# Kernel tuning notes

Measured on AMD Instinct MI355X. Metric: run time of the kernel, lower is better.

## Reference

```python
import jax, jax.numpy as jnp
import numpy as np

# --- fan-beam (flat detector) FBP geometry constants, matching init geo dict ---
V, U = 720, 736            # sino_views, nDetecU
NX = NY = 512              # nVoxelX, nVoxelY
SVOX = 400.0               # sVoxelX = sVoxelY (mm)
DU = 1.2858                # dDetecU (mm)
DSO, DOD = 595.0, 490.6    # source-origin, origin-detector distances
DSD = DSO + DOD
DBETA = 2.0 * np.pi / V    # angular step (full 2*pi scan, endpoint=False)


def _ramp_filter_fft():
    """Ram-Lak ramp filter (Kak & Slaney discrete spatial kernel), FFT'd for fast conv."""
    n = np.arange(-(U - 1), U)
    h = np.zeros(2 * U - 1, np.float64)
    h[U - 1] = 1.0 / (4.0 * DU * DU)
    odd = (np.abs(n) % 2 == 1)
    h[odd] = -1.0 / (np.pi * n[odd] * DU) ** 2
    L = int(2 ** np.ceil(np.log2(2 * (2 * U - 1))))  # zero-pad length (linear conv)
    return jnp.asarray(np.fft.fft(h, L).astype(np.complex64)), L

_HF, _L = _ramp_filter_fft()


def setup_inputs() -> dict:
    key = jax.random.key(0)
    sinogram = jax.random.uniform(key, (1, 1, V, U), dtype=jnp.float32)
    return {"sinogram": sinogram}


def reference(sinogram):
    # --- 1) cosine weighting of each detector sample ---
    sino = sinogram.reshape(V, U)
    us = (jnp.arange(U, dtype=jnp.float32) - (U - 1) / 2.0) * DU  # detector coords
    sino_w = sino * (DSD / jnp.sqrt(DSD * DSD + us * us))

    # --- 2) Ram-Lak ramp filtering per view (FFT linear convolution) ---
    Qf = jnp.fft.ifft(jnp.fft.fft(sino_w, n=_L, axis=1) * _HF[None, :], axis=1)
    Q = (jnp.real(Qf)[:, U - 1:2 * U - 1] * DU).astype(jnp.float32)  # [V, U]

    # --- 3) weighted fan-beam backprojection (scan over angles, O(Nx*Ny) carry) ---
    dx = SVOX / NX
    xs = (jnp.arange(NX, dtype=jnp.float32) - (NX - 1) / 2.0) * dx
    X, Y = jnp.meshgrid(xs, xs, indexing='ij')  # [NX, NY]
    betas = jnp.linspace(0.0, 2.0 * np.pi, V, endpoint=False).astype(jnp.float32)

    def body(img, ang_q):
        beta, q = ang_q                       # q: filtered projection [U]
        cb, sb = jnp.cos(beta), jnp.sin(beta)
        t = X * cb + Y * sb                   # coord along detector direction
        s = -X * sb + Y * cb                  # coord toward source
        D = DSO - s                           # source-to-pixel axial distance
        u = DSD * t / D                       # flat-detector intersection (mm)
        idx = u / DU + (U - 1) / 2.0          # fractional detector index
        i0 = jnp.clip(jnp.floor(idx), 0, U - 2).astype(jnp.int32)
        f = idx - i0
        val = q[i0] * (1.0 - f) + q[i0 + 1] * f
        val = jnp.where((idx >= 0.0) & (idx <= U - 1.0), val, 0.0)
        return img + (DSO / D) ** 2 * val, None

    img0 = jnp.zeros((NX, NY), jnp.float32)
    img, _ = jax.lax.scan(body, img0, (betas, Q))
    # 0.5 factor: full 2*pi fan scan covers each ray twice
    return (img * (0.5 * DBETA)).reshape(1, 1, NX, NY)
```

## Files before the change

kernel.cpp:

```cpp
#include <hip/hip_runtime.h>
#include <math.h>

#define NV 720
#define NU 736
#define NUP 768
#define NXY 512

__global__ __launch_bounds__(512) void filter_kernel(const float* __restrict__ sino,
                                                     float* __restrict__ Qi,
                                                     float4* __restrict__ trig,
                                                     float* __restrict__ out_zero) {
    __shared__ float s4[2][368][4];
    __shared__ float wco[736];
    __shared__ float part[3][128][8];
    const int bx = blockIdx.x;
    const int q = bx & 3;
    const int vb = bx >> 2;
    const int v0 = vb * 4;
    const int tid = threadIdx.x;
    const int tz = tid >> 7;
    const int J0 = tid & 127;

    for (int i = bx * 512 + tid; i < NXY * NXY; i += 720 * 512)
        out_zero[i] = 0.0f;

    if (q == 0 && tid < 4) {
        int v = v0 + tid;
        float beta = (float)((double)v * (2.0 * M_PI / 720.0));
        float cb = cosf(beta), sb = sinf(beta);
        const float K = (float)(1085.6 / 1.2858);
        trig[v] = make_float4(cb * K, sb * K, cb, sb);
    }
    const float DSD2 = (float)(1085.6 * 1085.6);
    for (int i = tid; i < 4 * NU; i += 512) {
        const int vv = i / NU, u = i - vv * NU;
        float us = ((float)u - 367.5f) * 1.2858f;
        float cw = 1085.6f / sqrtf(DSD2 + us * us);
        s4[u & 1][u >> 1][vv] = sino[(v0 + vv) * NU + u] * cw;
    }
    for (int i = tid; i < 736; i += 512) {
        double n = (double)(2 * i - 735);
        double a = M_PI * n * 1.2858;
        wco[i] = (float)(-1.0 / (a * a));
    }
    __syncthreads();

    const int m0 = 92 * tz;
    float a00 = 0.f, a01 = 0.f, a02 = 0.f, a03 = 0.f;
    float a10 = 0.f, a11 = 0.f, a12 = 0.f, a13 = 0.f;
    const int J0c = min(J0, 91);
    const int y0 = J0c + 367 + 92 * q;
    const float* wp = &wco[y0 - m0];

    #pragma unroll 4
    for (int mm = 0; mm < 92; ++mm) {
        const int m = m0 + mm;
        const float w0 = wp[-mm];
        const float w1 = wp[1 - mm];
        const float4 sv1 = *(const float4*)&s4[1][m][0];
        const float4 sv0 = *(const float4*)&s4[0][m][0];
        a00 = fmaf(w0, sv1.x, a00); a01 = fmaf(w0, sv1.y, a01);
        a02 = fmaf(w0, sv1.z, a02); a03 = fmaf(w0, sv1.w, a03);
        a10 = fmaf(w1, sv0.x, a10); a11 = fmaf(w1, sv0.y, a11);
        a12 = fmaf(w1, sv0.z, a12); a13 = fmaf(w1, sv0.w, a13);
    }

    if (tz != 0 && J0 < 92) {
        *(float4*)&part[tz - 1][J0][0] = make_float4(a00, a01, a02, a03);
        *(float4*)&part[tz - 1][J0][4] = make_float4(a10, a11, a12, a13);
    }
    __syncthreads();

    if (tz == 0 && J0 < 92) {
        #pragma unroll
        for (int g = 0; g < 3; ++g) {
            const float4 p0 = *(const float4*)&part[g][J0][0];
            const float4 p1 = *(const float4*)&part[g][J0][4];
            a00 += p0.x; a01 += p0.y; a02 += p0.z; a03 += p0.w;
            a10 += p1.x; a11 += p1.y; a12 += p1.z; a13 += p1.w;
        }
        const float H0 = (float)(1.0 / (4.0 * 1.2858 * 1.2858));
        const int mc = J0 + 92 * q;
        const float4 c0 = *(const float4*)&s4[0][mc][0];
        const float4 c1 = *(const float4*)&s4[1][mc][0];
        a00 = fmaf(H0, c0.x, a00); a01 = fmaf(H0, c0.y, a01);
        a02 = fmaf(H0, c0.z, a02); a03 = fmaf(H0, c0.w, a03);
        a10 = fmaf(H0, c1.x, a10); a11 = fmaf(H0, c1.y, a11);
        a12 = fmaf(H0, c1.z, a12); a13 = fmaf(H0, c1.w, a13);
        const int j0i = 2 * mc;
        const float DU = 1.2858f;
        const int v180 = v0 % 180;
        const int wq = v0 / 180;
        float* qr = Qi + (size_t)v180 * 3840 + wq;
        qr[0 * 3840 + 5 * j0i]     = a00 * DU;  qr[0 * 3840 + 5 * j0i + 5] = a10 * DU;
        qr[1 * 3840 + 5 * j0i]     = a01 * DU;  qr[1 * 3840 + 5 * j0i + 5] = a11 * DU;
        qr[2 * 3840 + 5 * j0i]     = a02 * DU;  qr[2 * 3840 + 5 * j0i + 5] = a12 * DU;
        qr[3 * 3840 + 5 * j0i]     = a03 * DU;  qr[3 * 3840 + 5 * j0i + 5] = a13 * DU;
    }
}

__global__ __launch_bounds__(256) void bp_kernel(const float* __restrict__ Qi,
                                                 const float4* __restrict__ trig,
                                                 float* __restrict__ out) {
    __shared__ float win[2][3840];
    const int b = blockIdx.x;
    const int c = b & 15;
    const int blk = b >> 4;
    const int bx = blk >> 4;
    const int by = blk & 15;
    const int t = threadIdx.x;
    const int w = t >> 6;
    const int l = t & 63;
    const int iq = (bx << 4) + ((w >> 1) << 3) + (l >> 3);
    const int jq = (by << 4) + ((w & 1) << 3) + (l & 7);

    const float dx = 400.0f / 512.0f;
    const float X = ((float)iq - 255.5f) * dx;
    const float Y = ((float)jq - 255.5f) * dx;
    const float Kc = (float)(1085.6 / 1.2858);

    float acc0 = 0.0f, acc1 = 0.0f, acc2 = 0.0f, acc3 = 0.0f;
    const bool inr = fmaf(X, X, Y * Y) <= 236.5f * 236.5f;
    const bool myint = __all(inr);

    const int nk = (c < 4) ? 12 : 11;
    const float* rowp = Qi + (size_t)c * 3840;
    const float4* tvp = trig + c;

    #pragma unroll
    for (int r = 0; r < 3; ++r)
        __builtin_amdgcn_global_load_lds(
            (const __attribute__((address_space(1))) void*)(rowp + r * 1024 + t * 4),
            (__attribute__((address_space(3))) void*)&win[0][r * 1024 + t * 4],
            16, 0, 0);
    if (w < 3)
        __builtin_amdgcn_global_load_lds(
            (const __attribute__((address_space(1))) void*)(rowp + 3072 + t * 4),
            (__attribute__((address_space(3))) void*)&win[0][3072 + t * 4],
            16, 0, 0);

    for (int it = 0; it < nk; ++it) {
        __syncthreads();
        if (it + 1 < nk) {
            const float* rn = rowp + 16 * 3840;
            float* wn = &win[(it + 1) & 1][0];
            #pragma unroll
            for (int r = 0; r < 3; ++r)
                __builtin_amdgcn_global_load_lds(
                    (const __attribute__((address_space(1))) void*)(rn + r * 1024 + t * 4),
                    (__attribute__((address_space(3))) void*)&wn[r * 1024 + t * 4],
                    16, 0, 0);
            if (w < 3)
                __builtin_amdgcn_global_load_lds(
                    (const __attribute__((address_space(1))) void*)(rn + 3072 + t * 4),
                    (__attribute__((address_space(3))) void*)&wn[3072 + t * 4],
                    16, 0, 0);
        }
        const float* winf = &win[it & 1][0];

        __builtin_amdgcn_s_setprio(1);
        if (myint) {
            const float4 tv = tvp[0];
            float a = fmaf(tv.z, X, tv.w * Y);
            float bb = fmaf(tv.z, Y, -tv.w * X);
            float aK = a * Kc, bK = bb * Kc;
            float D0 = 595.0f - bb, D1 = 595.0f + a, D2 = 595.0f + bb, D3 = 595.0f - a;
            float r0 = __builtin_amdgcn_rcpf(D0);
            float r1 = __builtin_amdgcn_rcpf(D1);
            float r2 = __builtin_amdgcn_rcpf(D2);
            float r3 = __builtin_amdgcn_rcpf(D3);
            float fi0 = fmaf(aK,  r0, 367.5f);
            float fi1 = fmaf(bK,  r1, 367.5f);
            float fi2 = fmaf(-aK, r2, 367.5f);
            float fi3 = fmaf(-bK, r3, 367.5f);
            int im[4] = {(int)fi0, (int)fi1, (int)fi2, (int)fi3};
            float ff[4] = {__builtin_amdgcn_fractf(fi0), __builtin_amdgcn_fractf(fi1),
                           __builtin_amdgcn_fractf(fi2), __builtin_amdgcn_fractf(fi3)};
            float gg[4] = {r0 * r0, r1 * r1, r2 * r2, r3 * r3};
            float* accp[4] = {&acc0, &acc1, &acc2, &acc3};
            #pragma unroll
            for (int m = 0; m < 4; ++m) {
                const float* pm = winf + 5 * im[m];
                #pragma unroll
                for (int k = 0; k < 4; ++k) {
                    float q0 = pm[k];
                    float q1 = pm[k + 5];
                    float val = fmaf(ff[m], q1 - q0, q0);
                    *accp[(m - k) & 3] = fmaf(gg[m], val, *accp[(m - k) & 3]);
                }
            }
        } else {
            const float4 tvs[4] = {tvp[0], tvp[180], tvp[360], tvp[540]};
            const float pX[4] = {X, Y, -X, -Y};
            const float pY[4] = {Y, -X, -Y, X};
            float* accp[4] = {&acc0, &acc1, &acc2, &acc3};
            #pragma unroll
            for (int j = 0; j < 4; ++j) {
                float Xm = pX[j], Ym = pY[j];
                #pragma unroll
                for (int k = 0; k < 4; ++k) {
                    const float4 tv = tvs[k];
                    float t2 = fmaf(tv.x, Xm, tv.y * Ym);
                    float D  = fmaf(tv.w, Xm, fmaf(tv.z, -Ym, 595.0f));
                    float rD = __builtin_amdgcn_rcpf(D);
                    float fidx = fmaf(t2, rD, 367.5f);
                    int i0c = min(max((int)fidx, 0), NU - 2);
                    float f = __builtin_amdgcn_fractf(fidx);
                    const float* pe = winf + 5 * i0c;
                    float q0 = pe[k];
                    float q1 = pe[k + 5];
                    float val = fmaf(f, q1 - q0, q0);
                    float cen = fidx - 367.5f;
                    float g = (__builtin_fabsf(cen) <= 367.5f) ? rD * rD : 0.0f;
                    *accp[j] = fmaf(g, val, *accp[j]);
                }
            }
        }
        __builtin_amdgcn_s_setprio(0);
        rowp += 16 * 3840;
        tvp += 16;
    }
    const float SC = (float)(595.0 * 595.0 * 0.5 * (2.0 * M_PI / 720.0));
    const int ir = 511 - iq, jr = 511 - jq;
    unsafeAtomicAdd(&out[iq * NXY + jq], acc0 * SC);
    unsafeAtomicAdd(&out[jq * NXY + ir], acc1 * SC);
    unsafeAtomicAdd(&out[ir * NXY + jr], acc2 * SC);
    unsafeAtomicAdd(&out[jr * NXY + iq], acc3 * SC);
}

extern "C" void kernel_launch(void* const* d_in, const int* in_sizes, int n_in,
                              void* d_out, int out_size, void* d_ws, size_t ws_size,
                              hipStream_t stream) {
    const float* sino = (const float*)d_in[0];
    float* out = (float*)d_out;
    float* Qi = (float*)d_ws;
    float4* trig = (float4*)((char*)d_ws + (size_t)180 * 3840 * sizeof(float));

    filter_kernel<<<720, 512, 0, stream>>>(sino, Qi, trig, out);
    bp_kernel<<<4096, 256, 0, stream>>>(Qi, trig, out);
}
```

Before: 111.1 us.

## Repack interleaved projection rows to stride-4 layout with duplicated group boundaries

Changes the per-detector interleave of four symmetric views from a stride-5 padded layout to a stride-4 layout with one duplicated entry every 8 detector bins. The backprojection inner loop can then fetch both interpolation neighbours as two aligned float4 LDS reads instead of eight scalar reads. The filter kernel writes the extra boundary copies, the row size shrinks so less data is staged into LDS, and the edge path is reordered to compute indices first and gather afterwards. The cost is extra index arithmetic (e + e>>3) and a more intricate layout that must stay consistent between the two kernels.

```diff
diff --git a/kernel.cpp b/kernel.cpp
--- a/kernel.cpp
+++ b/kernel.cpp
@@ -3,8 +3,9 @@
 
 #define NV 720
 #define NU 736
-#define NUP 768
 #define NXY 512
+#define WROW 3312
+#define WPAD 3328
 
 __global__ __launch_bounds__(512) void filter_kernel(const float* __restrict__ sino,
                                                      float* __restrict__ Qi,
@@ -87,22 +88,29 @@
         a02 = fmaf(H0, c0.z, a02); a03 = fmaf(H0, c0.w, a03);
         a10 = fmaf(H0, c1.x, a10); a11 = fmaf(H0, c1.y, a11);
         a12 = fmaf(H0, c1.z, a12); a13 = fmaf(H0, c1.w, a13);
+        const float DU = 1.2858f;
         const int j0i = 2 * mc;
-        const float DU = 1.2858f;
         const int v180 = v0 % 180;
         const int wq = v0 / 180;
-        float* qr = Qi + (size_t)v180 * 3840 + wq;
-        qr[0 * 3840 + 5 * j0i]     = a00 * DU;  qr[0 * 3840 + 5 * j0i + 5] = a10 * DU;
-        qr[1 * 3840 + 5 * j0i]     = a01 * DU;  qr[1 * 3840 + 5 * j0i + 5] = a11 * DU;
-        qr[2 * 3840 + 5 * j0i]     = a02 * DU;  qr[2 * 3840 + 5 * j0i + 5] = a12 * DU;
-        qr[3 * 3840 + 5 * j0i]     = a03 * DU;  qr[3 * 3840 + 5 * j0i + 5] = a13 * DU;
+        const int d0 = 4 * (j0i + (j0i >> 3)) + wq;
+        float* qr = Qi + (size_t)v180 * WROW;
+        qr[0 * WROW + d0] = a00 * DU;  qr[0 * WROW + d0 + 4] = a10 * DU;
+        qr[1 * WROW + d0] = a01 * DU;  qr[1 * WROW + d0 + 4] = a11 * DU;
+        qr[2 * WROW + d0] = a02 * DU;  qr[2 * WROW + d0 + 4] = a12 * DU;
+        qr[3 * WROW + d0] = a03 * DU;  qr[3 * WROW + d0 + 4] = a13 * DU;
+        if (j0i && !(j0i & 7)) {
+            qr[0 * WROW + d0 - 4] = a00 * DU;
+            qr[1 * WROW + d0 - 4] = a01 * DU;
+            qr[2 * WROW + d0 - 4] = a02 * DU;
+            qr[3 * WROW + d0 - 4] = a03 * DU;
+        }
     }
 }
 
 __global__ __launch_bounds__(256) void bp_kernel(const float* __restrict__ Qi,
                                                  const float4* __restrict__ trig,
                                                  float* __restrict__ out) {
-    __shared__ float win[2][3840];
+    __shared__ __align__(16) float win[2][WPAD];
     const int b = blockIdx.x;
     const int c = b & 15;
     const int blk = b >> 4;
@@ -124,7 +132,7 @@
     const bool myint = __all(inr);
 
     const int nk = (c < 4) ? 12 : 11;
-    const float* rowp = Qi + (size_t)c * 3840;
+    const float* rowp = Qi + (size_t)c * WROW;
     const float4* tvp = trig + c;
 
     #pragma unroll
@@ -133,16 +141,16 @@
             (const __attribute__((address_space(1))) void*)(rowp + r * 1024 + t * 4),
             (__attribute__((address_space(3))) void*)&win[0][r * 1024 + t * 4],
             16, 0, 0);
-    if (w < 3)
+    if (w == 0)
         __builtin_amdgcn_global_load_lds(
-            (const __attribute__((address_space(1))) void*)(rowp + 3072 + t * 4),
-            (__attribute__((address_space(3))) void*)&win[0][3072 + t * 4],
+            (const __attribute__((address_space(1))) void*)(rowp + 3072 + l * 4),
+            (__attribute__((address_space(3))) void*)&win[0][3072 + l * 4],
             16, 0, 0);
 
     for (int it = 0; it < nk; ++it) {
         __syncthreads();
         if (it + 1 < nk) {
-            const float* rn = rowp + 16 * 3840;
+            const float* rn = rowp + 16 * WROW;
             float* wn = &win[(it + 1) & 1][0];
             #pragma unroll
             for (int r = 0; r < 3; ++r)
@@ -150,10 +158,10 @@
                     (const __attribute__((address_space(1))) void*)(rn + r * 1024 + t * 4),
                     (__attribute__((address_space(3))) void*)&wn[r * 1024 + t * 4],
                     16, 0, 0);
-            if (w < 3)
+            if (w == 0)
                 __builtin_amdgcn_global_load_lds(
-                    (const __attribute__((address_space(1))) void*)(rn + 3072 + t * 4),
-                    (__attribute__((address_space(3))) void*)&wn[3072 + t * 4],
+                    (const __attribute__((address_space(1))) void*)(rn + 3072 + l * 4),
+                    (__attribute__((address_space(3))) void*)&wn[3072 + l * 4],
                     16, 0, 0);
         }
         const float* winf = &win[it & 1][0];
@@ -180,12 +188,15 @@
             float* accp[4] = {&acc0, &acc1, &acc2, &acc3};
             #pragma unroll
             for (int m = 0; m < 4; ++m) {
-                const float* pm = winf + 5 * im[m];
+                const int e = im[m] + (im[m] >> 3);
+                const float* pm = winf + 4 * e;
+                const float4 qa = *(const float4*)pm;
+                const float4 qb = *(const float4*)(pm + 4);
+                const float qa_[4] = {qa.x, qa.y, qa.z, qa.w};
+                const float qb_[4] = {qb.x, qb.y, qb.z, qb.w};
                 #pragma unroll
                 for (int k = 0; k < 4; ++k) {
-                    float q0 = pm[k];
-                    float q1 = pm[k + 5];
-                    float val = fmaf(ff[m], q1 - q0, q0);
+                    float val = fmaf(ff[m], qb_[k] - qa_[k], qa_[k]);
                     *accp[(m - k) & 3] = fmaf(gg[m], val, *accp[(m - k) & 3]);
                 }
             }
@@ -195,29 +206,35 @@
             const float pY[4] = {Y, -X, -Y, X};
             float* accp[4] = {&acc0, &acc1, &acc2, &acc3};
             #pragma unroll
-            for (int j = 0; j < 4; ++j) {
-                float Xm = pX[j], Ym = pY[j];
+            for (int k = 0; k < 4; ++k) {
+                const float4 tv = tvs[k];
+                float fx[4], gx[4];
+                int ic[4];
                 #pragma unroll
-                for (int k = 0; k < 4; ++k) {
-                    const float4 tv = tvs[k];
+                for (int j = 0; j < 4; ++j) {
+                    float Xm = pX[j], Ym = pY[j];
                     float t2 = fmaf(tv.x, Xm, tv.y * Ym);
                     float D  = fmaf(tv.w, Xm, fmaf(tv.z, -Ym, 595.0f));
                     float rD = __builtin_amdgcn_rcpf(D);
                     float fidx = fmaf(t2, rD, 367.5f);
-                    int i0c = min(max((int)fidx, 0), NU - 2);
-                    float f = __builtin_amdgcn_fractf(fidx);
-                    const float* pe = winf + 5 * i0c;
+                    ic[j] = min(max((int)fidx, 0), NU - 2);
+                    fx[j] = __builtin_amdgcn_fractf(fidx);
+                    float cen = fidx - 367.5f;
+                    gx[j] = (__builtin_fabsf(cen) <= 367.5f) ? rD * rD : 0.0f;
+                }
+                #pragma unroll
+                for (int j = 0; j < 4; ++j) {
+                    const int e = ic[j] + (ic[j] >> 3);
+                    const float* pe = winf + 4 * e;
                     float q0 = pe[k];
-                    float q1 = pe[k + 5];
-                    float val = fmaf(f, q1 - q0, q0);
-                    float cen = fidx - 367.5f;
-                    float g = (__builtin_fabsf(cen) <= 367.5f) ? rD * rD : 0.0f;
-                    *accp[j] = fmaf(g, val, *accp[j]);
+                    float q1 = pe[k + 4];
+                    float val = fmaf(fx[j], q1 - q0, q0);
+                    *accp[j] = fmaf(gx[j], val, *accp[j]);
                 }
             }
         }
         __builtin_amdgcn_s_setprio(0);
-        rowp += 16 * 3840;
+        rowp += 16 * WROW;
         tvp += 16;
     }
     const float SC = (float)(595.0 * 595.0 * 0.5 * (2.0 * M_PI / 720.0));
@@ -234,7 +251,7 @@
     const float* sino = (const float*)d_in[0];
     float* out = (float*)d_out;
     float* Qi = (float*)d_ws;
-    float4* trig = (float4*)((char*)d_ws + (size_t)180 * 3840 * sizeof(float));
+    float4* trig = (float4*)((char*)d_ws + (size_t)180 * WROW * sizeof(float));
 
     filter_kernel<<<720, 512, 0, stream>>>(sino, Qi, trig, out);
     bp_kernel<<<4096, 256, 0, stream>>>(Qi, trig, out);
```

New measurement: 114.3 us. +2.9%, slower.
